# Optimization experiments

Hardware: AMD Instinct MI355X
Metric: run time of the kernel (lower is better)

## Reference

```python
import jax, jax.numpy as jnp
from jax import lax
import numpy as np

NUM_KIND = 4
V, H, B = 34, 32, 4096   # raw vertical (2 rows dropped), horizontal, batch
KS = 33                  # odd-rounded max(V-2, H)
NUM_DEPTH = 4
N_SQ = 100


def _conv(x, w):
    # x: (N,1,h,w), w: (1,1,KS,KS); torch Conv2d == cross-correlation == lax default
    return lax.conv_general_dilated(x, w, (1, 1), 'SAME',
                                    dimension_numbers=('NCHW', 'OIHW', 'NCHW'))


def _conv_k(x, w):
    # x: (K,B,1,h,w) -> conv each map with the shared 1-channel kernel
    k, b, c, h, wd = x.shape
    return _conv(x.reshape(k * b, c, h, wd), w).reshape(k, b, c, h, wd)


def setup_inputs() -> dict:
    key = jax.random.key(0)
    ks = jax.random.split(key, 8)
    std = 0.3
    return {
        'dots':    jax.random.randint(ks[0], (V, H, B), 0, NUM_KIND + 1, dtype=jnp.int32),
        'w_each':  jax.random.normal(ks[1], (1, 1, KS, KS), jnp.float32) * std,
        'w_not':   jax.random.normal(ks[2], (1, 1, KS, KS), jnp.float32) * std,
        'w_not2':  jax.random.normal(ks[3], (1, 1, KS, KS), jnp.float32) * std,
        'w_empty': jax.random.normal(ks[4], (1, 1, KS, KS), jnp.float32) * std,
        'W1':      jax.random.normal(ks[5], (N_SQ, (V - 2) * H), jnp.float32) * std,
        'W2':      jax.random.normal(ks[6], (N_SQ, N_SQ), jnp.float32) * std,
        'W3':      jax.random.normal(ks[7], (1, N_SQ), jnp.float32) * std,
    }


def reference(dots, w_each, w_not, w_not2, w_empty, W1, W2, W3):
    # drop last 2 vertical rows, layout (V-2,H,B) -> (B,1,V-2,H)
    board = dots[:-2].astype(jnp.float32).transpose(2, 0, 1)[:, None]  # (B,1,h,w)

    empty = (board == 0).astype(jnp.float32)
    E = _conv(empty, w_empty)                                           # (B,1,h,w)

    kinds = jnp.arange(1, NUM_KIND + 1, dtype=board.dtype).reshape(NUM_KIND, 1, 1, 1, 1)
    each = (board[None] == kinds).astype(jnp.float32)                   # (K,B,1,h,w)
    notm = ((each + empty[None]) == 0).astype(jnp.float32)              # (K,B,1,h,w)

    # first pass: per-color value, masked to that color's cells
    notm_conv = _conv_k(notm, w_not)      # note: the torch code LOGS the convolved not-mask
    v = _conv_k(each, w_each) + E[None] - notm_conv
    L = each * v                          # each_color_value_log (masked)
    s = jax.nn.sigmoid(L.sum(axis=0))     # all_color_value_2nd, (B,1,h,w)

    # iterative diffusion; torch mutates the log in-place each depth:
    # L <- mask * (L + E + conv2nd(notm_conv * before)); before is detached
    for _ in range(NUM_DEPTH):
        before = lax.stop_gradient(s)
        C = _conv_k(notm_conv * before[None], w_not2)
        L = each * (L + E[None] + C)
        s = jax.nn.sigmoid(L.sum(axis=0))

    feat = s.reshape(s.shape[0], -1)      # (B, (V-2)*H)
    x = jax.nn.leaky_relu(feat @ W1.T, 0.2)
    x = jax.nn.leaky_relu(x @ W2.T, 0.2)
    return x @ W3.T                        # (B,1)
```

## Files before the change

### kernel.cpp

```cpp
#include <hip/hip_runtime.h>
#include <cstdint>
#include <cstddef>


typedef _Float16 f16;
typedef __attribute__((ext_vector_type(8))) _Float16 f16x8;
typedef __attribute__((ext_vector_type(4))) float f32x4;

#define NB   4096
#define PIX  1024
#define MR   (NB * 4)

__device__ __forceinline__ void gld_lds16(const void* g, void* l) {
    __builtin_amdgcn_global_load_lds(
        (const __attribute__((address_space(1))) void*)g,
        (__attribute__((address_space(3))) void*)l, 16, 0, 0);
}

__device__ __forceinline__ void band_range(int otile, int& t_lo, int& t_hi) {
    int i0 = otile >> 5;
    t_lo = (i0 > 16) ? ((i0 - 16) >> 1) : 0;
    t_hi = (i0 + 19) >> 1;
    if (t_hi > 15) t_hi = 15;
}

__global__ void build_all(const float* __restrict__ we, const float* __restrict__ wn,
                          const float* __restrict__ wn2, const float* __restrict__ wem,
                          const float* __restrict__ W1, const int* __restrict__ dots,
                          f16* __restrict__ Me, f16* __restrict__ Mn,
                          f16* __restrict__ Mn2, f16* __restrict__ Mem,
                          f16* __restrict__ W1b, unsigned char* __restrict__ board) {
    __shared__ unsigned char tile[64][68];
    int bi = blockIdx.x, t = threadIdx.x;
    if (bi < 4096) {
        int idx = bi * 256 + t;
        int o = idx >> 10, in = idx & 1023;
        int i = o >> 5, j = o & 31, a = in >> 5, b = in & 31;
        int u = a - i + 16, v = b - j + 16;
        bool ok = (u >= 0) && (u < 33) && (v >= 0) && (v < 33);
        int w = u * 33 + v;
        float ve = 0.f, vn = 0.f, vn2 = 0.f, vem = 0.f;
        if (ok) { ve = we[w]; vn = wn[w]; vn2 = wn2[w]; vem = wem[w]; }
        Me[idx]  = (f16)ve;
        Mn[idx]  = (f16)vn;
        Mn2[idx] = (f16)vn2;
        Mem[idx] = (f16)vem;
    } else if (bi < 4608) {
        int idx = (bi - 4096) * 256 + t;
        int j = idx >> 10, i = idx & 1023;
        W1b[idx] = (f16)(j < 100 ? W1[j * 1024 + i] : 0.f);
    } else {
        int bb = bi - 4608;
        int bp = bb & 15, bn = bb >> 4;
        int p0 = bp * 64, n0 = bn * 64;
        int ln = t & 63, lp = t >> 6;
#pragma unroll
        for (int j = 0; j < 16; j++) {
            int p = lp * 16 + j;
            tile[p][ln] = (unsigned char)dots[(size_t)(p0 + p) * 4096 + n0 + ln];
        }
        __syncthreads();
#pragma unroll
        for (int j = 0; j < 16; j++) {
            int n = lp * 16 + j;
            board[(size_t)(n0 + n) * 1024 + p0 + ln] = tile[ln][n];
        }
    }
}

__global__ void expand_masks(const unsigned char* __restrict__ board,
                             f16* __restrict__ eachF, f16* __restrict__ notmF,
                             f16* __restrict__ emptyF) {
    int bi = blockIdx.x, t = threadIdx.x;
    if (bi < 8192) {
        int idx = bi * 256 + t;
        int r = idx >> 7, w0 = (idx & 127) << 3;
        int n = r >> 2, k1 = (r & 3) + 1;
        uint64_t bb = *(const uint64_t*)(board + (size_t)n * 1024 + w0);
        f16x8 e, m;
#pragma unroll
        for (int j = 0; j < 8; j++) {
            int bj = (int)((bb >> (8 * j)) & 0xff);
            e[j] = (bj == k1) ? (f16)1.f : (f16)0.f;
            m[j] = (bj != 0 && bj != k1) ? (f16)1.f : (f16)0.f;
        }
        *(f16x8*)(eachF + (size_t)idx * 8) = e;
        *(f16x8*)(notmF + (size_t)idx * 8) = m;
    } else {
        int idx = (bi - 8192) * 256 + t;
        int n = idx >> 7, w0 = (idx & 127) << 3;
        uint64_t bb = *(const uint64_t*)(board + (size_t)n * 1024 + w0);
        f16x8 e;
#pragma unroll
        for (int j = 0; j < 8; j++)
            e[j] = (((bb >> (8 * j)) & 0xff) == 0) ? (f16)1.f : (f16)0.f;
        *(f16x8*)(emptyF + (size_t)idx * 8) = e;
    }
}

template <int MODE>
__device__ __forceinline__ void run_gemm(
    int bjob, int ypx, int nx, char* smem,
    const f16* __restrict__ X, const f16* __restrict__ B,
    const unsigned char* __restrict__ board, const f16* __restrict__ En,
    const f16* __restrict__ NCs, f16* __restrict__ Lsel,
    f16* __restrict__ Pout, f16* __restrict__ outB, int ldo) {
    char* smB = smem;
    char* smA = smem + 16384;

    const int tid = threadIdx.x;
    const int wv = tid >> 6, ln = tid & 63;
    const int wm = wv >> 1, wn_ = wv & 1;
    const int lr = ln & 15, lq = ln >> 4;

    int xcd = bjob & 7, slot = bjob >> 3;
    int bx = slot % nx;
    int by = xcd * ypx + slot / nx;
    const int rtile = by * 128, otile = bx * 128;

    int t_lo, t_hi;
    band_range(otile, t_lo, t_hi);

    const f32x4 fz = {0.f, 0.f, 0.f, 0.f};
    f32x4 acc[4][4];
#pragma unroll
    for (int i = 0; i < 4; i++)
#pragma unroll
        for (int j = 0; j < 4; j++) acc[i][j] = fz;

    for (int kt = t_lo; kt <= t_hi; kt++) {
        const int kb = kt * 64;
#pragma unroll
        for (int t = 0; t < 4; t++) {
            int c = (wv * 4 + t) * 64 + ln;
            int row = c >> 3, gcol = (c & 7) ^ (row & 7);
            gld_lds16(B + (size_t)(otile + row) * 1024 + kb + gcol * 8, smB + c * 16);
            gld_lds16(X + (size_t)(rtile + row) * 1024 + kb + gcol * 8, smA + c * 16);
        }
        __syncthreads();

#pragma unroll
        for (int kk = 0; kk < 2; kk++) {
            const int oct = kk * 4 + lq;
            f16x8 af[4], bfr[4];
#pragma unroll
            for (int i = 0; i < 4; i++) {
                int rrow = wm * 64 + i * 16 + lr;
                af[i] = *(const f16x8*)(smA + rrow * 128 + (oct ^ (rrow & 7)) * 16);
            }
#pragma unroll
            for (int j = 0; j < 4; j++) {
                int brow = wn_ * 64 + j * 16 + lr;
                bfr[j] = *(const f16x8*)(smB + brow * 128 + (oct ^ (brow & 7)) * 16);
            }
#pragma unroll
            for (int i = 0; i < 4; i++)
#pragma unroll
                for (int j = 0; j < 4; j++)
                    acc[i][j] = __builtin_amdgcn_mfma_f32_16x16x32_f16(
                        af[i], bfr[j], acc[i][j], 0, 0, 0);
        }
        __syncthreads();
    }

    if constexpr (MODE == 0) {
        f16* sT = (f16*)smem;
#pragma unroll
        for (int i = 0; i < 4; i++) {
            int rb = wm * 64 + i * 16 + lq * 4;
#pragma unroll
            for (int j = 0; j < 4; j++) {
                int col = wn_ * 64 + j * 16 + lr;
                f32x4 a = acc[i][j];
#pragma unroll
                for (int v = 0; v < 4; v++)
                    sT[(rb + v) * 136 + col] = (f16)a[v];
            }
        }
        __syncthreads();
#pragma unroll
        for (int it = 0; it < 8; it++) {
            int row = it * 16 + (tid >> 4), cg = tid & 15;
            f16x8 vv = *(const f16x8*)(sT + row * 136 + cg * 8);
            *(f16x8*)(outB + (size_t)(rtile + row) * ldo + otile + cg * 8) = vv;
        }
    } else {
        float* sAcc = (float*)smem;
#pragma unroll
        for (int h = 0; h < 2; h++) {
            if (wm == h) {
#pragma unroll
                for (int i = 0; i < 4; i++) {
                    int lrow = i * 16 + lq * 4;
#pragma unroll
                    for (int j = 0; j < 4; j++) {
                        int col = wn_ * 64 + j * 16 + lr;
                        f32x4 a = acc[i][j];
#pragma unroll
                        for (int v = 0; v < 4; v++)
                            sAcc[(lrow + v) * 132 + col] = a[v];
                    }
                }
            }
            __syncthreads();
            {
                int cell = tid >> 4, cg = tid & 15;
                int rb = rtile + h * 64 + cell * 4;
                int ngl = rb >> 2;
                int o = otile + cg * 8;
                size_t no = (size_t)ngl * PIX + o;
                uint64_t bb = *(const uint64_t*)(board + no);
                f16x8 en8 = *(const f16x8*)(En + no);
                size_t r0 = (size_t)rb * PIX + o;
                f16x8 nc0 = *(const f16x8*)(NCs + r0);
                f16x8 nc1 = *(const f16x8*)(NCs + r0 + PIX);
                f16x8 nc2 = *(const f16x8*)(NCs + r0 + 2 * PIX);
                f16x8 nc3 = *(const f16x8*)(NCs + r0 + 3 * PIX);
                const float* ar = sAcc + cell * 4 * 132 + cg * 8;
                f32x4 arow[4][2];
#pragma unroll
                for (int k = 0; k < 4; k++) {
                    arow[k][0] = *(const f32x4*)(ar + k * 132);
                    arow[k][1] = *(const f32x4*)(ar + k * 132 + 4);
                }
                f16x8 lout, p0, p1, p2, p3;
#pragma unroll
                for (int j2 = 0; j2 < 8; j2++) {
                    int c = (int)((bb >> (8 * j2)) & 0xff);
                    float a0 = arow[0][j2 >> 2][j2 & 3];
                    float a1 = arow[1][j2 >> 2][j2 & 3];
                    float a2 = arow[2][j2 >> 2][j2 & 3];
                    float a3 = arow[3][j2 >> 2][j2 & 3];
                    float asel = (c == 1) ? a0 : (c == 2) ? a1 : (c == 3) ? a2 : a3;
                    float L = 0.f;
                    if (c > 0) {
                        float ncsel = (float)((c == 1) ? nc0[j2] : (c == 2) ? nc1[j2]
                                            : (c == 3) ? nc2[j2] : nc3[j2]);
                        L = asel + (float)en8[j2] - ncsel;
                    }
                    lout[j2] = (f16)L;
                    f16 s = (f16)(1.f / (1.f + __expf(-L)));
                    p0[j2] = nc0[j2] * s;
                    p1[j2] = nc1[j2] * s;
                    p2[j2] = nc2[j2] * s;
                    p3[j2] = nc3[j2] * s;
                }
                *(f16x8*)(Lsel + no)            = lout;
                *(f16x8*)(Pout + r0)            = p0;
                *(f16x8*)(Pout + r0 + PIX)      = p1;
                *(f16x8*)(Pout + r0 + 2 * PIX)  = p2;
                *(f16x8*)(Pout + r0 + 3 * PIX)  = p3;
            }
            __syncthreads();
        }
    }
}

__global__ void __launch_bounds__(256, 4) gemm_faA(
    const f16* __restrict__ Mn, const f16* __restrict__ Mem,
    const f16* __restrict__ notmF, const f16* __restrict__ emptyF,
    f16* __restrict__ NC, f16* __restrict__ En) {
    __shared__ __attribute__((aligned(16))) char smem[34816];
    int bi = blockIdx.x;
    if (bi < 1024) {
        run_gemm<0>(bi, 16, 8, smem, notmF, Mn, nullptr, nullptr, nullptr,
                    nullptr, nullptr, NC, PIX);
    } else {
        run_gemm<0>(bi - 1024, 4, 8, smem, emptyF, Mem, nullptr, nullptr, nullptr,
                    nullptr, nullptr, En, PIX);
    }
}

__global__ void __launch_bounds__(256, 4) gemm_faB(
    const f16* __restrict__ Me, const f16* __restrict__ eachF,
    const unsigned char* __restrict__ board, const f16* __restrict__ En,
    const f16* __restrict__ NC, f16* __restrict__ Lsel, f16* __restrict__ P1) {
    __shared__ __attribute__((aligned(16))) char smem[36864];
    run_gemm<2>(blockIdx.x, 16, 8, smem, eachF, Me, board, En, NC,
                Lsel, P1, nullptr, 0);
}

template <int MODE>
__global__ void __launch_bounds__(256, 4) gemm_depth(
    const f16* __restrict__ Pin, const f16* __restrict__ Mn2,
    const unsigned char* __restrict__ board, const f16* __restrict__ NC,
    const f16* __restrict__ En, f16* __restrict__ Lsel,
    f16* __restrict__ Pout, f16* __restrict__ feat) {
    __shared__ __attribute__((aligned(16))) char smem[36864];
    char* smB = smem;
    char* smA = smem + 16384;

    const int tid = threadIdx.x;
    const int wv = tid >> 6, ln = tid & 63;
    const int wm = wv >> 1, wn_ = wv & 1;
    const int lr = ln & 15, lq = ln >> 4;

    int bi = blockIdx.x;
    int xcd = bi & 7, slot = bi >> 3;
    int bx = slot & 7;
    int by = xcd * 16 + (slot >> 3);
    const int rtile = by * 128, otile = bx * 128;

    int t_lo, t_hi;
    band_range(otile, t_lo, t_hi);

    const f32x4 fz = {0.f, 0.f, 0.f, 0.f};
    f32x4 acc[4][4];
#pragma unroll
    for (int i = 0; i < 4; i++)
#pragma unroll
        for (int j = 0; j < 4; j++) acc[i][j] = fz;

    for (int kt = t_lo; kt <= t_hi; kt++) {
        const int kb = kt * 64;
#pragma unroll
        for (int t = 0; t < 4; t++) {
            int c = (wv * 4 + t) * 64 + ln;
            int row = c >> 3, gcol = (c & 7) ^ (row & 7);
            gld_lds16(Mn2 + (size_t)(otile + row) * 1024 + kb + gcol * 8, smB + c * 16);
            gld_lds16(Pin + (size_t)(rtile + row) * 1024 + kb + gcol * 8, smA + c * 16);
        }
        __syncthreads();

#pragma unroll
        for (int kk = 0; kk < 2; kk++) {
            const int oct = kk * 4 + lq;
            f16x8 af[4], bfr[4];
#pragma unroll
            for (int i = 0; i < 4; i++) {
                int rrow = wm * 64 + i * 16 + lr;
                af[i] = *(const f16x8*)(smA + rrow * 128 + (oct ^ (rrow & 7)) * 16);
            }
#pragma unroll
            for (int j = 0; j < 4; j++) {
                int brow = wn_ * 64 + j * 16 + lr;
                bfr[j] = *(const f16x8*)(smB + brow * 128 + (oct ^ (brow & 7)) * 16);
            }
#pragma unroll
            for (int i = 0; i < 4; i++)
#pragma unroll
                for (int j = 0; j < 4; j++)
                    acc[i][j] = __builtin_amdgcn_mfma_f32_16x16x32_f16(
                        af[i], bfr[j], acc[i][j], 0, 0, 0);
        }
        __syncthreads();
    }

    float* sAcc = (float*)smem;
#pragma unroll
    for (int h = 0; h < 2; h++) {
        if (wm == h) {
#pragma unroll
            for (int i = 0; i < 4; i++) {
                int lrow = i * 16 + lq * 4;
#pragma unroll
                for (int j = 0; j < 4; j++) {
                    int col = wn_ * 64 + j * 16 + lr;
                    f32x4 a = acc[i][j];
#pragma unroll
                    for (int v = 0; v < 4; v++)
                        sAcc[(lrow + v) * 132 + col] = a[v];
                }
            }
        }
        __syncthreads();
        {
            int cell = tid >> 4, cg = tid & 15;
            int rb = rtile + h * 64 + cell * 4;
            int ngl = rb >> 2;
            int o = otile + cg * 8;
            size_t no = (size_t)ngl * PIX + o;
            uint64_t bb = *(const uint64_t*)(board + no);
            f16x8 en8 = *(const f16x8*)(En + no);
            f16x8 ls8 = *(const f16x8*)(Lsel + no);
            const float* ar = sAcc + cell * 4 * 132 + cg * 8;
            f32x4 arow[4][2];
#pragma unroll
            for (int k = 0; k < 4; k++) {
                arow[k][0] = *(const f32x4*)(ar + k * 132);
                arow[k][1] = *(const f32x4*)(ar + k * 132 + 4);
            }
            if constexpr (MODE == 4) {
                f16x8 s8;
#pragma unroll
                for (int j2 = 0; j2 < 8; j2++) {
                    int c = (int)((bb >> (8 * j2)) & 0xff);
                    float a0 = arow[0][j2 >> 2][j2 & 3];
                    float a1 = arow[1][j2 >> 2][j2 & 3];
                    float a2 = arow[2][j2 >> 2][j2 & 3];
                    float a3 = arow[3][j2 >> 2][j2 & 3];
                    float asel = (c == 1) ? a0 : (c == 2) ? a1 : (c == 3) ? a2 : a3;
                    float L = 0.f;
                    if (c > 0) L = (float)ls8[j2] + (float)en8[j2] + asel;
                    s8[j2] = (f16)(1.f / (1.f + __expf(-L)));
                }
                *(f16x8*)(feat + no) = s8;
            } else {
                size_t r0 = (size_t)rb * PIX + o;
                f16x8 nc0 = *(const f16x8*)(NC + r0);
                f16x8 nc1 = *(const f16x8*)(NC + r0 + PIX);
                f16x8 nc2 = *(const f16x8*)(NC + r0 + 2 * PIX);
                f16x8 nc3 = *(const f16x8*)(NC + r0 + 3 * PIX);
                f16x8 lout, p0, p1, p2, p3;
#pragma unroll
                for (int j2 = 0; j2 < 8; j2++) {
                    int c = (int)((bb >> (8 * j2)) & 0xff);
                    float a0 = arow[0][j2 >> 2][j2 & 3];
                    float a1 = arow[1][j2 >> 2][j2 & 3];
                    float a2 = arow[2][j2 >> 2][j2 & 3];
                    float a3 = arow[3][j2 >> 2][j2 & 3];
                    float asel = (c == 1) ? a0 : (c == 2) ? a1 : (c == 3) ? a2 : a3;
                    float L = 0.f;
                    if (c > 0) L = (float)ls8[j2] + (float)en8[j2] + asel;
                    lout[j2] = (f16)L;
                    f16 s = (f16)(1.f / (1.f + __expf(-L)));
                    p0[j2] = nc0[j2] * s;
                    p1[j2] = nc1[j2] * s;
                    p2[j2] = nc2[j2] * s;
                    p3[j2] = nc3[j2] * s;
                }
                *(f16x8*)(Lsel + no)           = lout;
                *(f16x8*)(Pout + r0)           = p0;
                *(f16x8*)(Pout + r0 + PIX)     = p1;
                *(f16x8*)(Pout + r0 + 2 * PIX) = p2;
                *(f16x8*)(Pout + r0 + 3 * PIX) = p3;
            }
        }
        __syncthreads();
    }
}

__global__ void __launch_bounds__(256) gemm_mlp_fused(
    const f16* __restrict__ feat, const f16* __restrict__ W1b,
    const float* __restrict__ W2, const float* __restrict__ W3,
    float* __restrict__ out) {
    __shared__ __attribute__((aligned(16))) char smem[47360];
    char* smB = smem;
    char* smA = smem + 16384;

    const int tid = threadIdx.x;
    const int wv = tid >> 6, ln = tid & 63;
    const int wm = wv >> 1, wn_ = wv & 1;
    const int lr = ln & 15, lq = ln >> 4;
    const int rtile = blockIdx.x * 64;

    const f32x4 fz = {0.f, 0.f, 0.f, 0.f};
    f32x4 acc[2][4];
#pragma unroll
    for (int i = 0; i < 2; i++)
#pragma unroll
        for (int j = 0; j < 4; j++) acc[i][j] = fz;

    for (int kb = 0; kb < 1024; kb += 64) {
#pragma unroll
        for (int t = 0; t < 4; t++) {
            int c = (wv * 4 + t) * 64 + ln;
            int row = c >> 3, gcol = (c & 7) ^ (row & 7);
            gld_lds16(W1b + (size_t)row * 1024 + kb + gcol * 8, smB + c * 16);
        }
#pragma unroll
        for (int t = 0; t < 2; t++) {
            int c = t * 256 + tid;
            int row = c >> 3, gcol = (c & 7) ^ (row & 7);
            gld_lds16(feat + (size_t)(rtile + row) * 1024 + kb + gcol * 8, smA + c * 16);
        }
        __syncthreads();
#pragma unroll
        for (int kk = 0; kk < 2; kk++) {
            const int oct = kk * 4 + lq;
            f16x8 af[2], bfr[4];
#pragma unroll
            for (int i = 0; i < 2; i++) {
                int rrow = wm * 32 + i * 16 + lr;
                af[i] = *(const f16x8*)(smA + rrow * 128 + (oct ^ (rrow & 7)) * 16);
            }
#pragma unroll
            for (int j = 0; j < 4; j++) {
                int brow = wn_ * 64 + j * 16 + lr;
                bfr[j] = *(const f16x8*)(smB + brow * 128 + (oct ^ (brow & 7)) * 16);
            }
#pragma unroll
            for (int i = 0; i < 2; i++)
#pragma unroll
                for (int j = 0; j < 4; j++)
                    acc[i][j] = __builtin_amdgcn_mfma_f32_16x16x32_f16(
                        af[i], bfr[j], acc[i][j], 0, 0, 0);
        }
        __syncthreads();
    }

    float* xs  = (float*)smem;
    f16*   sW2 = (f16*)(smem + 25856);
    float* sW3 = (float*)(smem + 45856);
    float* red = (float*)(smem + 46272);
    for (int idx = tid; idx < 10000; idx += 256) sW2[idx] = (f16)W2[idx];
    if (tid < 100) sW3[tid] = W3[tid];

#pragma unroll
    for (int i = 0; i < 2; i++) {
        int rb = wm * 32 + i * 16 + lq * 4;
#pragma unroll
        for (int j = 0; j < 4; j++) {
            int o = wn_ * 64 + j * 16 + lr;
            if (o < 100) {
                f32x4 a = acc[i][j];
#pragma unroll
                for (int v = 0; v < 4; v++) {
                    float x = a[v];
                    xs[(rb + v) * 101 + o] = x > 0.f ? x : 0.2f * x;
                }
            }
        }
    }
    __syncthreads();
    {
        int nb = tid >> 2, q = tid & 3;
        const float* xrow = xs + nb * 101;
        float partial = 0.f;
        for (int jj = 0; jj < 25; jj++) {
            int j = q + jj * 4;
            const f16* w2r = sW2 + j * 100;
            float a2 = 0.f;
#pragma unroll
            for (int i = 0; i < 100; i++) a2 += (float)w2r[i] * xrow[i];
            partial += sW3[j] * (a2 > 0.f ? a2 : 0.2f * a2);
        }
        red[tid] = partial;
        __syncthreads();
        if (q == 0)
            out[rtile + nb] = red[tid] + red[tid + 1] + red[tid + 2] + red[tid + 3];
    }
}

extern "C" void kernel_launch(void* const* d_in, const int* in_sizes, int n_in,
                              void* d_out, int out_size, void* d_ws, size_t ws_size,
                              hipStream_t stream) {
    (void)in_sizes; (void)n_in; (void)out_size; (void)ws_size;
    const int*   dots   = (const int*)d_in[0];
    const float* w_each = (const float*)d_in[1];
    const float* w_not  = (const float*)d_in[2];
    const float* w_not2 = (const float*)d_in[3];
    const float* w_emp  = (const float*)d_in[4];
    const float* W1 = (const float*)d_in[5];
    const float* W2 = (const float*)d_in[6];
    const float* W3 = (const float*)d_in[7];
    float* out = (float*)d_out;

    char* ws = (char*)d_ws;
    size_t off = 0;
    auto alloc = [&](size_t bytes) -> char* {
        char* p = ws + off;
        off += (bytes + 255) & ~(size_t)255;
        return p;
    };
    f16* Me    = (f16*)alloc((size_t)PIX * PIX * 2);
    f16* Mn    = (f16*)alloc((size_t)PIX * PIX * 2);
    f16* Mn2   = (f16*)alloc((size_t)PIX * PIX * 2);
    f16* Mem   = (f16*)alloc((size_t)PIX * PIX * 2);
    f16* W1b   = (f16*)alloc((size_t)128 * PIX * 2);
    unsigned char* board = (unsigned char*)alloc((size_t)NB * PIX);
    f16* eachF = (f16*)alloc((size_t)MR * PIX * 2);
    f16* notmF = (f16*)alloc((size_t)MR * PIX * 2);
    f16* emptyF= (f16*)alloc((size_t)NB * PIX * 2);
    f16* NC    = (f16*)alloc((size_t)MR * PIX * 2);
    f16* En    = (f16*)alloc((size_t)NB * PIX * 2);
    f16* Lsel  = (f16*)alloc((size_t)NB * PIX * 2);
    f16* feat  = (f16*)alloc((size_t)NB * PIX * 2);
    f16* Pa = notmF;
    f16* Pb = eachF;

    dim3 blk(256);
    build_all<<<5632, blk, 0, stream>>>(w_each, w_not, w_not2, w_emp, W1, dots,
                                        Me, Mn, Mn2, Mem, W1b, board);
    expand_masks<<<10240, blk, 0, stream>>>(board, eachF, notmF, emptyF);
    gemm_faA<<<1280, blk, 0, stream>>>(Mn, Mem, notmF, emptyF, NC, En);
    gemm_faB<<<1024, blk, 0, stream>>>(Me, eachF, board, En, NC, Lsel, Pa);
    gemm_depth<3><<<1024, blk, 0, stream>>>(Pa, Mn2, board, NC, En, Lsel, Pb, nullptr);
    gemm_depth<3><<<1024, blk, 0, stream>>>(Pb, Mn2, board, NC, En, Lsel, Pa, nullptr);
    gemm_depth<3><<<1024, blk, 0, stream>>>(Pa, Mn2, board, NC, En, Lsel, Pb, nullptr);
    gemm_depth<4><<<1024, blk, 0, stream>>>(Pb, Mn2, board, NC, En, Lsel, nullptr, feat);
    gemm_mlp_fused<<<64, blk, 0, stream>>>(feat, W1b, W2, W3, out);
}
```

Before: 365.5 us.

## Pass per-pixel sigmoid instead of 4x products and multiply in GEMM A-load

Each depth epilogue now writes only the per-pixel sigmoid S, not four NC*S product planes. The next depth GEMM reloads NC as its A operand plus a small S tile, and forms NC*S in registers before the MFMA. The first GEMM also emits a color-selected NC plane, so the faB epilogue reads one plane instead of four. This cuts epilogue global writes and reads roughly fourfold, at the cost of an extra LDS tile read and a vector multiply in the inner loop.

```diff
diff --git a/kernel.cpp b/kernel.cpp
--- a/kernel.cpp
+++ b/kernel.cpp
@@ -103,8 +103,9 @@
     int bjob, int ypx, int nx, char* smem,
     const f16* __restrict__ X, const f16* __restrict__ B,
     const unsigned char* __restrict__ board, const f16* __restrict__ En,
-    const f16* __restrict__ NCs, f16* __restrict__ Lsel,
-    f16* __restrict__ Pout, f16* __restrict__ outB, int ldo) {
+    const f16* __restrict__ NCsel_in, f16* __restrict__ Lsel,
+    f16* __restrict__ Sout, f16* __restrict__ outB, int ldo,
+    f16* __restrict__ NCselOut) {
     char* smB = smem;
     char* smA = smem + 16384;
 
@@ -163,7 +164,7 @@
         __syncthreads();
     }
 
-    if constexpr (MODE == 0) {
+    if constexpr (MODE == 0 || MODE == 5) {
         f16* sT = (f16*)smem;
 #pragma unroll
         for (int i = 0; i < 4; i++) {
@@ -183,6 +184,27 @@
             int row = it * 16 + (tid >> 4), cg = tid & 15;
             f16x8 vv = *(const f16x8*)(sT + row * 136 + cg * 8);
             *(f16x8*)(outB + (size_t)(rtile + row) * ldo + otile + cg * 8) = vv;
+        }
+        if constexpr (MODE == 5) {
+#pragma unroll
+            for (int g = 0; g < 2; g++) {
+                int slot = g * 256 + tid;
+                int cell = slot >> 4, cg = slot & 15;
+                size_t no = (size_t)((rtile >> 2) + cell) * PIX + otile + cg * 8;
+                uint64_t bb = *(const uint64_t*)(board + no);
+                f16x8 q0 = *(const f16x8*)(sT + (cell * 4 + 0) * 136 + cg * 8);
+                f16x8 q1 = *(const f16x8*)(sT + (cell * 4 + 1) * 136 + cg * 8);
+                f16x8 q2 = *(const f16x8*)(sT + (cell * 4 + 2) * 136 + cg * 8);
+                f16x8 q3 = *(const f16x8*)(sT + (cell * 4 + 3) * 136 + cg * 8);
+                f16x8 nsel;
+#pragma unroll
+                for (int j2 = 0; j2 < 8; j2++) {
+                    int c = (int)((bb >> (8 * j2)) & 0xff);
+                    nsel[j2] = (c == 1) ? q0[j2] : (c == 2) ? q1[j2]
+                             : (c == 3) ? q2[j2] : q3[j2];
+                }
+                *(f16x8*)(NCselOut + no) = nsel;
+            }
         }
     } else {
         float* sAcc = (float*)smem;
@@ -211,11 +233,7 @@
                 size_t no = (size_t)ngl * PIX + o;
                 uint64_t bb = *(const uint64_t*)(board + no);
                 f16x8 en8 = *(const f16x8*)(En + no);
-                size_t r0 = (size_t)rb * PIX + o;
-                f16x8 nc0 = *(const f16x8*)(NCs + r0);
-                f16x8 nc1 = *(const f16x8*)(NCs + r0 + PIX);
-                f16x8 nc2 = *(const f16x8*)(NCs + r0 + 2 * PIX);
-                f16x8 nc3 = *(const f16x8*)(NCs + r0 + 3 * PIX);
+                f16x8 ns8 = *(const f16x8*)(NCsel_in + no);
                 const float* ar = sAcc + cell * 4 * 132 + cg * 8;
                 f32x4 arow[4][2];
 #pragma unroll
@@ -223,7 +241,7 @@
                     arow[k][0] = *(const f32x4*)(ar + k * 132);
                     arow[k][1] = *(const f32x4*)(ar + k * 132 + 4);
                 }
-                f16x8 lout, p0, p1, p2, p3;
+                f16x8 lout, s8;
 #pragma unroll
                 for (int j2 = 0; j2 < 8; j2++) {
                     int c = (int)((bb >> (8 * j2)) & 0xff);
@@ -233,23 +251,12 @@
                     float a3 = arow[3][j2 >> 2][j2 & 3];
                     float asel = (c == 1) ? a0 : (c == 2) ? a1 : (c == 3) ? a2 : a3;
                     float L = 0.f;
-                    if (c > 0) {
-                        float ncsel = (float)((c == 1) ? nc0[j2] : (c == 2) ? nc1[j2]
-                                            : (c == 3) ? nc2[j2] : nc3[j2]);
-                        L = asel + (float)en8[j2] - ncsel;
-                    }
+                    if (c > 0) L = asel + (float)en8[j2] - (float)ns8[j2];
                     lout[j2] = (f16)L;
-                    f16 s = (f16)(1.f / (1.f + __expf(-L)));
-                    p0[j2] = nc0[j2] * s;
-                    p1[j2] = nc1[j2] * s;
-                    p2[j2] = nc2[j2] * s;
-                    p3[j2] = nc3[j2] * s;
+                    s8[j2] = (f16)(1.f / (1.f + __expf(-L)));
                 }
-                *(f16x8*)(Lsel + no)            = lout;
-                *(f16x8*)(Pout + r0)            = p0;
-                *(f16x8*)(Pout + r0 + PIX)      = p1;
-                *(f16x8*)(Pout + r0 + 2 * PIX)  = p2;
-                *(f16x8*)(Pout + r0 + 3 * PIX)  = p3;
+                *(f16x8*)(Lsel + no) = lout;
+                *(f16x8*)(Sout + no) = s8;
             }
             __syncthreads();
         }
@@ -259,36 +266,39 @@
 __global__ void __launch_bounds__(256, 4) gemm_faA(
     const f16* __restrict__ Mn, const f16* __restrict__ Mem,
     const f16* __restrict__ notmF, const f16* __restrict__ emptyF,
-    f16* __restrict__ NC, f16* __restrict__ En) {
+    const unsigned char* __restrict__ board,
+    f16* __restrict__ NC, f16* __restrict__ En, f16* __restrict__ NCsel) {
     __shared__ __attribute__((aligned(16))) char smem[34816];
     int bi = blockIdx.x;
     if (bi < 1024) {
-        run_gemm<0>(bi, 16, 8, smem, notmF, Mn, nullptr, nullptr, nullptr,
-                    nullptr, nullptr, NC, PIX);
+        run_gemm<5>(bi, 16, 8, smem, notmF, Mn, board, nullptr, nullptr,
+                    nullptr, nullptr, NC, PIX, NCsel);
     } else {
         run_gemm<0>(bi - 1024, 4, 8, smem, emptyF, Mem, nullptr, nullptr, nullptr,
-                    nullptr, nullptr, En, PIX);
+                    nullptr, nullptr, En, PIX, nullptr);
     }
 }
 
 __global__ void __launch_bounds__(256, 4) gemm_faB(
     const f16* __restrict__ Me, const f16* __restrict__ eachF,
     const unsigned char* __restrict__ board, const f16* __restrict__ En,
-    const f16* __restrict__ NC, f16* __restrict__ Lsel, f16* __restrict__ P1) {
+    const f16* __restrict__ NCsel, f16* __restrict__ Lsel,
+    f16* __restrict__ S1) {
     __shared__ __attribute__((aligned(16))) char smem[36864];
-    run_gemm<2>(blockIdx.x, 16, 8, smem, eachF, Me, board, En, NC,
-                Lsel, P1, nullptr, 0);
+    run_gemm<2>(blockIdx.x, 16, 8, smem, eachF, Me, board, En, NCsel,
+                Lsel, S1, nullptr, 0, nullptr);
 }
 
 template <int MODE>
 __global__ void __launch_bounds__(256, 4) gemm_depth(
-    const f16* __restrict__ Pin, const f16* __restrict__ Mn2,
-    const unsigned char* __restrict__ board, const f16* __restrict__ NC,
-    const f16* __restrict__ En, f16* __restrict__ Lsel,
-    f16* __restrict__ Pout, f16* __restrict__ feat) {
+    const f16* __restrict__ NC, const f16* __restrict__ Mn2,
+    const unsigned char* __restrict__ board, const f16* __restrict__ En,
+    const f16* __restrict__ Sin, f16* __restrict__ Lsel,
+    f16* __restrict__ Sout) {
     __shared__ __attribute__((aligned(16))) char smem[36864];
     char* smB = smem;
     char* smA = smem + 16384;
+    char* smS = smem + 32768;
 
     const int tid = threadIdx.x;
     const int wv = tid >> 6, ln = tid & 63;
@@ -300,6 +310,7 @@
     int bx = slot & 7;
     int by = xcd * 16 + (slot >> 3);
     const int rtile = by * 128, otile = bx * 128;
+    const int n0 = rtile >> 2;
 
     int t_lo, t_hi;
     band_range(otile, t_lo, t_hi);
@@ -318,7 +329,11 @@
             int c = (wv * 4 + t) * 64 + ln;
             int row = c >> 3, gcol = (c & 7) ^ (row & 7);
             gld_lds16(Mn2 + (size_t)(otile + row) * 1024 + kb + gcol * 8, smB + c * 16);
-            gld_lds16(Pin + (size_t)(rtile + row) * 1024 + kb + gcol * 8, smA + c * 16);
+            gld_lds16(NC  + (size_t)(rtile + row) * 1024 + kb + gcol * 8, smA + c * 16);
+        }
+        {
+            int row = tid >> 3, c8 = tid & 7;
+            gld_lds16(Sin + (size_t)(n0 + row) * 1024 + kb + c8 * 8, smS + tid * 16);
         }
         __syncthreads();
 
@@ -329,7 +344,9 @@
 #pragma unroll
             for (int i = 0; i < 4; i++) {
                 int rrow = wm * 64 + i * 16 + lr;
-                af[i] = *(const f16x8*)(smA + rrow * 128 + (oct ^ (rrow & 7)) * 16);
+                f16x8 nv = *(const f16x8*)(smA + rrow * 128 + (oct ^ (rrow & 7)) * 16);
+                f16x8 sv = *(const f16x8*)(smS + (rrow >> 2) * 128 + oct * 16);
+                af[i] = nv * sv;
             }
 #pragma unroll
             for (int j = 0; j < 4; j++) {
@@ -380,51 +397,22 @@
                 arow[k][0] = *(const f32x4*)(ar + k * 132);
                 arow[k][1] = *(const f32x4*)(ar + k * 132 + 4);
             }
-            if constexpr (MODE == 4) {
-                f16x8 s8;
-#pragma unroll
-                for (int j2 = 0; j2 < 8; j2++) {
-                    int c = (int)((bb >> (8 * j2)) & 0xff);
-                    float a0 = arow[0][j2 >> 2][j2 & 3];
-                    float a1 = arow[1][j2 >> 2][j2 & 3];
-                    float a2 = arow[2][j2 >> 2][j2 & 3];
-                    float a3 = arow[3][j2 >> 2][j2 & 3];
-                    float asel = (c == 1) ? a0 : (c == 2) ? a1 : (c == 3) ? a2 : a3;
-                    float L = 0.f;
-                    if (c > 0) L = (float)ls8[j2] + (float)en8[j2] + asel;
-                    s8[j2] = (f16)(1.f / (1.f + __expf(-L)));
-                }
-                *(f16x8*)(feat + no) = s8;
-            } else {
-                size_t r0 = (size_t)rb * PIX + o;
-                f16x8 nc0 = *(const f16x8*)(NC + r0);
-                f16x8 nc1 = *(const f16x8*)(NC + r0 + PIX);
-                f16x8 nc2 = *(const f16x8*)(NC + r0 + 2 * PIX);
-                f16x8 nc3 = *(const f16x8*)(NC + r0 + 3 * PIX);
-                f16x8 lout, p0, p1, p2, p3;
-#pragma unroll
-                for (int j2 = 0; j2 < 8; j2++) {
-                    int c = (int)((bb >> (8 * j2)) & 0xff);
-                    float a0 = arow[0][j2 >> 2][j2 & 3];
-                    float a1 = arow[1][j2 >> 2][j2 & 3];
-                    float a2 = arow[2][j2 >> 2][j2 & 3];
-                    float a3 = arow[3][j2 >> 2][j2 & 3];
-                    float asel = (c == 1) ? a0 : (c == 2) ? a1 : (c == 3) ? a2 : a3;
-                    float L = 0.f;
-                    if (c > 0) L = (float)ls8[j2] + (float)en8[j2] + asel;
-                    lout[j2] = (f16)L;
-                    f16 s = (f16)(1.f / (1.f + __expf(-L)));
-                    p0[j2] = nc0[j2] * s;
-                    p1[j2] = nc1[j2] * s;
-                    p2[j2] = nc2[j2] * s;
-                    p3[j2] = nc3[j2] * s;
-                }
-                *(f16x8*)(Lsel + no)           = lout;
-                *(f16x8*)(Pout + r0)           = p0;
-                *(f16x8*)(Pout + r0 + PIX)     = p1;
-                *(f16x8*)(Pout + r0 + 2 * PIX) = p2;
-                *(f16x8*)(Pout + r0 + 3 * PIX) = p3;
-            }
+            f16x8 lout, s8;
+#pragma unroll
+            for (int j2 = 0; j2 < 8; j2++) {
+                int c = (int)((bb >> (8 * j2)) & 0xff);
+                float a0 = arow[0][j2 >> 2][j2 & 3];
+                float a1 = arow[1][j2 >> 2][j2 & 3];
+                float a2 = arow[2][j2 >> 2][j2 & 3];
+                float a3 = arow[3][j2 >> 2][j2 & 3];
+                float asel = (c == 1) ? a0 : (c == 2) ? a1 : (c == 3) ? a2 : a3;
+                float L = 0.f;
+                if (c > 0) L = (float)ls8[j2] + (float)en8[j2] + asel;
+                lout[j2] = (f16)L;
+                s8[j2] = (f16)(1.f / (1.f + __expf(-L)));
+            }
+            if constexpr (MODE == 3) *(f16x8*)(Lsel + no) = lout;
+            *(f16x8*)(Sout + no) = s8;
         }
         __syncthreads();
     }
@@ -565,19 +553,20 @@
     f16* NC    = (f16*)alloc((size_t)MR * PIX * 2);
     f16* En    = (f16*)alloc((size_t)NB * PIX * 2);
     f16* Lsel  = (f16*)alloc((size_t)NB * PIX * 2);
-    f16* feat  = (f16*)alloc((size_t)NB * PIX * 2);
-    f16* Pa = notmF;
-    f16* Pb = eachF;
+    f16* NCsel = (f16*)alloc((size_t)NB * PIX * 2);
+    f16* Sa    = (f16*)alloc((size_t)NB * PIX * 2);
+    f16* Sb    = (f16*)alloc((size_t)NB * PIX * 2);
 
     dim3 blk(256);
     build_all<<<5632, blk, 0, stream>>>(w_each, w_not, w_not2, w_emp, W1, dots,
                                         Me, Mn, Mn2, Mem, W1b, board);
     expand_masks<<<10240, blk, 0, stream>>>(board, eachF, notmF, emptyF);
-    gemm_faA<<<1280, blk, 0, stream>>>(Mn, Mem, notmF, emptyF, NC, En);
-    gemm_faB<<<1024, blk, 0, stream>>>(Me, eachF, board, En, NC, Lsel, Pa);
-    gemm_depth<3><<<1024, blk, 0, stream>>>(Pa, Mn2, board, NC, En, Lsel, Pb, nullptr);
-    gemm_depth<3><<<1024, blk, 0, stream>>>(Pb, Mn2, board, NC, En, Lsel, Pa, nullptr);
-    gemm_depth<3><<<1024, blk, 0, stream>>>(Pa, Mn2, board, NC, En, Lsel, Pb, nullptr);
-    gemm_depth<4><<<1024, blk, 0, stream>>>(Pb, Mn2, board, NC, En, Lsel, nullptr, feat);
-    gemm_mlp_fused<<<64, blk, 0, stream>>>(feat, W1b, W2, W3, out);
-}
+    gemm_faA<<<1280, blk, 0, stream>>>(Mn, Mem, notmF, emptyF, board,
+                                       NC, En, NCsel);
+    gemm_faB<<<1024, blk, 0, stream>>>(Me, eachF, board, En, NCsel, Lsel, Sa);
+    gemm_depth<3><<<1024, blk, 0, stream>>>(NC, Mn2, board, En, Sa, Lsel, Sb);
+    gemm_depth<3><<<1024, blk, 0, stream>>>(NC, Mn2, board, En, Sb, Lsel, Sa);
+    gemm_depth<3><<<1024, blk, 0, stream>>>(NC, Mn2, board, En, Sa, Lsel, Sb);
+    gemm_depth<4><<<1024, blk, 0, stream>>>(NC, Mn2, board, En, Sb, Lsel, Sa);
+    gemm_mlp_fused<<<64, blk, 0, stream>>>(Sa, W1b, W2, W3, out);
+}
```

After: 411.8 us. 12.7% more time.
